# Optimization experiments

Hardware: AMD Instinct MI355X
Metric: run time of the kernel (lower is better)

The kernel has to match this reference:

```python
import jax, jax.numpy as jnp
import numpy as np

MARGIN = 0.5

def setup_inputs() -> dict:
    key = jax.random.key(0)
    k1, k2 = jax.random.split(key)
    n, d, n_classes = 8192, 512, 1024
    embedding = jax.random.normal(k1, (n, d), dtype=jnp.float32)
    label = jax.random.randint(k2, (n,), 0, n_classes, dtype=jnp.int64)
    return {"embedding": embedding, "label": label}


def reference(embedding, label):
    # sim_mat[i, j] = <e_i, e_j>
    n = embedding.shape[0]
    sim = embedding @ embedding.T  # [n, n]
    same = label[:, None] == label[None, :]  # [n, n] bool
    # per-row positive pairs: same label AND sim < 1; loss contrib (1 - sim)
    pos_mask = same & (sim < 1.0)
    # per-row negative pairs (hard mining): diff label AND sim > margin; loss contrib sim
    neg_mask = (~same) & (sim > MARGIN)
    pos_loss = jnp.sum(jnp.where(pos_mask, 1.0 - sim, 0.0))
    neg_loss = jnp.sum(jnp.where(neg_mask, sim, 0.0))
    loss = (pos_loss + neg_loss) / n
    return (loss, 0, 0)
```

## Files before the change

### kernel.cpp

```cpp
#include <hip/hip_runtime.h>
#include <hip/hip_bf16.h>


typedef int   i32x4 __attribute__((ext_vector_type(4)));
typedef float f32x4 __attribute__((ext_vector_type(4)));

#define N_EMB 8192
#define D_EMB 512
#define BM    128
#define HKB   64
#define NPH   (D_EMB / HKB)
#define TILES (N_EMB / BM)
#define NBLK  (TILES * (TILES + 1) / 2)
#define MARGIN_F 0.5f
#define QSCALE 24.0f
#define DEQ    (1.0f / (QSCALE * QSCALE))
#define HBYT  (BM * HKB)

__device__ __forceinline__ void gll16(const void* g, void* l) {
    __builtin_amdgcn_global_load_lds(
        (const __attribute__((address_space(1))) void*)g,
        (__attribute__((address_space(3))) void*)l,
        16 , 0 , 0 );
}

__global__ __launch_bounds__(256) void quant_kernel(const float* __restrict__ in,
                                                    int4* __restrict__ out, int n16) {
    int i = blockIdx.x * blockDim.x + threadIdx.x;
    if (i >= n16) return;
    const float4* p = reinterpret_cast<const float4*>(in) + i * 4;
    int4 o;
    int* po = reinterpret_cast<int*>(&o);
#pragma unroll
    for (int j = 0; j < 4; ++j) {
        float4 v = p[j];
        int b0 = (int)rintf(fminf(fmaxf(v.x * QSCALE, -127.f), 127.f));
        int b1 = (int)rintf(fminf(fmaxf(v.y * QSCALE, -127.f), 127.f));
        int b2 = (int)rintf(fminf(fmaxf(v.z * QSCALE, -127.f), 127.f));
        int b3 = (int)rintf(fminf(fmaxf(v.w * QSCALE, -127.f), 127.f));
        po[j] = (b0 & 255) | ((b1 & 255) << 8) | ((b2 & 255) << 16) | ((b3 & 255) << 24);
    }
    out[i] = o;
}

__global__ __launch_bounds__(256) void loss_kernel(const char* __restrict__ E8,
                                                   const int* __restrict__ label,
                                                   float* __restrict__ partials) {
    const int bid = blockIdx.x;
    const int t = (bid & 7) * (NBLK / 8) + (bid >> 3);

    int tr = (int)(64.5f - sqrtf(4160.25f - 2.0f * (float)t));
    while ((tr + 1) * TILES - ((tr + 1) * tr) / 2 <= t) ++tr;
    while (tr * TILES - (tr * (tr - 1)) / 2 > t) --tr;
    const int tc = tr + (t - (tr * TILES - (tr * (tr - 1)) / 2));

    __shared__ char  lds[3][2][HBYT];
    __shared__ float red[4];

    const int tid  = threadIdx.x;
    const int wid  = tid >> 6, lane = tid & 63;
    const int wrow = wid >> 1, wcol = wid & 1;
    const int fr   = lane & 15;
    const int kq   = lane >> 4;
    const int row0 = tr * BM, col0 = tc * BM;

    const int sw = (((tid & 3) ^ ((tid >> 2) & 3)) << 4);
    const int r0 = tid >> 2, r1 = 64 + (tid >> 2);
    const char* gA0 = E8 + (size_t)(row0 + r0) * D_EMB + sw;
    const char* gA1 = E8 + (size_t)(row0 + r1) * D_EMB + sw;
    const char* gB0 = E8 + (size_t)(col0 + r0) * D_EMB + sw;
    const char* gB1 = E8 + (size_t)(col0 + r1) * D_EMB + sw;
    const int d0 = tid << 4;
    const int d1 = (tid + 256) << 4;

    i32x4 acc[4][4] = {};

    const int psw = ((kq ^ (fr & 3)) << 4);

    gll16(gA0,       &lds[0][0][d0]); gll16(gA1,       &lds[0][0][d1]);
    gll16(gB0,       &lds[0][1][d0]); gll16(gB1,       &lds[0][1][d1]);
    gll16(gA0 + HKB, &lds[1][0][d0]); gll16(gA1 + HKB, &lds[1][0][d1]);
    gll16(gB0 + HKB, &lds[1][1][d0]); gll16(gB1 + HKB, &lds[1][1][d1]);
    asm volatile("s_waitcnt vmcnt(4)" ::: "memory");
    __builtin_amdgcn_s_barrier();

#pragma unroll
    for (int p = 0; p < NPH; ++p) {
        const int rg = p % 3;
        i32x4 a[4], b[4];
#pragma unroll
        for (int m = 0; m < 4; ++m)
            a[m] = *reinterpret_cast<const i32x4*>(
                &lds[rg][0][((wrow * 64 + m * 16 + fr) << 6) + psw]);
#pragma unroll
        for (int n = 0; n < 4; ++n)
            b[n] = *reinterpret_cast<const i32x4*>(
                &lds[rg][1][((wcol * 64 + n * 16 + fr) << 6) + psw]);
        if (p + 2 < NPH) {
            const int rg2 = (p + 2) % 3;
            const int ko  = (p + 2) * HKB;
            gll16(gA0 + ko, &lds[rg2][0][d0]); gll16(gA1 + ko, &lds[rg2][0][d1]);
            gll16(gB0 + ko, &lds[rg2][1][d0]); gll16(gB1 + ko, &lds[rg2][1][d1]);
        }
        if (p < NPH - 2) {
            asm volatile("s_waitcnt vmcnt(4)" ::: "memory");
        } else if (p == NPH - 2) {
            asm volatile("s_waitcnt vmcnt(0)" ::: "memory");
        }
        __builtin_amdgcn_s_barrier();
        asm volatile("s_waitcnt lgkmcnt(0)" ::: "memory");
        __builtin_amdgcn_sched_barrier(0);
        __builtin_amdgcn_s_setprio(1);
#pragma unroll
        for (int m = 0; m < 4; ++m)
#pragma unroll
            for (int n = 0; n < 4; ++n)
                acc[m][n] = __builtin_amdgcn_mfma_i32_16x16x64_i8(a[m], b[n], acc[m][n], 0, 0, 0);
        __builtin_amdgcn_s_setprio(0);
        __builtin_amdgcn_s_barrier();
    }

    float local = 0.f;
    int lj[4];
#pragma unroll
    for (int n = 0; n < 4; ++n) lj[n] = label[col0 + wcol * 64 + n * 16 + fr];
    const int rb = kq << 2;
#pragma unroll
    for (int m = 0; m < 4; ++m) {
#pragma unroll
        for (int r = 0; r < 4; ++r) {
            const int li = label[row0 + wrow * 64 + m * 16 + rb + r];
#pragma unroll
            for (int n = 0; n < 4; ++n) {
                const float s = (float)acc[m][n][r] * DEQ;
                if (li == lj[n]) {
                    if (s < 1.0f) local += 1.0f - s;
                } else if (s > MARGIN_F) {
                    local += s;
                }
            }
        }
    }
    if (tr != tc) local *= 2.0f;

#pragma unroll
    for (int off = 32; off > 0; off >>= 1) local += __shfl_xor(local, off);
    if (lane == 0) red[wid] = local;
    __syncthreads();
    if (tid == 0) partials[t] = red[0] + red[1] + red[2] + red[3];
}

__global__ __launch_bounds__(256) void reduce_kernel(const float* __restrict__ partials,
                                                     float* __restrict__ out, int nb) {
    float s = 0.f;
    for (int i = threadIdx.x; i < nb; i += 256) s += partials[i];
#pragma unroll
    for (int off = 32; off > 0; off >>= 1) s += __shfl_xor(s, off);
    __shared__ float red[4];
    if ((threadIdx.x & 63) == 0) red[threadIdx.x >> 6] = s;
    __syncthreads();
    if (threadIdx.x == 0) {
        out[0] = (red[0] + red[1] + red[2] + red[3]) * (1.0f / (float)N_EMB);
        out[1] = 0.f;
        out[2] = 0.f;
    }
}

extern "C" void kernel_launch(void* const* d_in, const int* in_sizes, int n_in,
                              void* d_out, int out_size, void* d_ws, size_t ws_size,
                              hipStream_t stream) {
    const float* emb   = (const float*)d_in[0];
    const int*   label = (const int*)d_in[1];
    float*       out   = (float*)d_out;

    char*  E8      = (char*)d_ws;
    float* partial = (float*)((char*)d_ws + (size_t)N_EMB * D_EMB);

    const int n16 = N_EMB * D_EMB / 16;
    quant_kernel<<<(n16 + 255) / 256, 256, 0, stream>>>(emb, (int4*)E8, n16);

    loss_kernel<<<NBLK, 256, 0, stream>>>(E8, label, partial);

    reduce_kernel<<<1, 256, 0, stream>>>(partial, out, NBLK);
}
```

Baseline: 46.15 us.

## Use 256x128 rectangular tiles with 512-thread blocks and per-element triangle masking

The loss kernel moves from square 128x128 upper-triangle tiles to 256-row by 128-column tiles run by 8 waves, with a new row/column tile mapping over the triangle. Each block loads a larger A panel that all 8 waves share, which cuts global and LDS load traffic per output element. Diagonal tiles are now handled by masking to gi<gj and doubling each term, instead of doubling whole off-diagonal tiles. This wastes some MFMA work on the partly covered diagonal tiles and drops the i==j terms, which only matters if a self-similarity is below 1. The larger LDS footprint may also lower occupancy.

New measurement: 47.26 us. 1.02x slower.

```diff
diff --git a/kernel.cpp b/kernel.cpp
--- a/kernel.cpp
+++ b/kernel.cpp
@@ -7,15 +7,18 @@
 
 #define N_EMB 8192
 #define D_EMB 512
-#define BM    128
+#define BMR   256
+#define BNC   128
 #define HKB   64
 #define NPH   (D_EMB / HKB)
-#define TILES (N_EMB / BM)
-#define NBLK  (TILES * (TILES + 1) / 2)
+#define RT    (N_EMB / BMR)
+#define CT    (N_EMB / BNC)
+#define NBLK  1056
 #define MARGIN_F 0.5f
 #define QSCALE 24.0f
 #define DEQ    (1.0f / (QSCALE * QSCALE))
-#define HBYT  (BM * HKB)
+#define ABYT  (BMR * HKB)
+#define BBYT  (BNC * HKB)
 
 __device__ __forceinline__ void gll16(const void* g, void* l) {
     __builtin_amdgcn_global_load_lds(
@@ -43,45 +46,46 @@
     out[i] = o;
 }
 
-__global__ __launch_bounds__(256) void loss_kernel(const char* __restrict__ E8,
+__global__ __launch_bounds__(512) void loss_kernel(const char* __restrict__ E8,
                                                    const int* __restrict__ label,
                                                    float* __restrict__ partials) {
     const int bid = blockIdx.x;
     const int t = (bid & 7) * (NBLK / 8) + (bid >> 3);
 
-    int tr = (int)(64.5f - sqrtf(4160.25f - 2.0f * (float)t));
-    while ((tr + 1) * TILES - ((tr + 1) * tr) / 2 <= t) ++tr;
-    while (tr * TILES - (tr * (tr - 1)) / 2 > t) --tr;
-    const int tc = tr + (t - (tr * TILES - (tr * (tr - 1)) / 2));
+    int R = (int)((65.0f - sqrtf(4225.0f - 4.0f * (float)t)) * 0.5f);
+    if (R < 0) R = 0; if (R > RT - 1) R = RT - 1;
+    while ((R + 1) * (65 - (R + 1)) <= t) ++R;
+    while (R * (65 - R) > t) --R;
+    const int C = 2 * R + (t - R * (65 - R));
 
-    __shared__ char  lds[3][2][HBYT];
-    __shared__ float red[4];
+    __shared__ char  lds[3][ABYT + BBYT];
+    __shared__ float red[8];
 
     const int tid  = threadIdx.x;
     const int wid  = tid >> 6, lane = tid & 63;
     const int wrow = wid >> 1, wcol = wid & 1;
     const int fr   = lane & 15;
     const int kq   = lane >> 4;
-    const int row0 = tr * BM, col0 = tc * BM;
+    const int row0 = R * BMR, col0 = C * BNC;
 
-    const int sw = (((tid & 3) ^ ((tid >> 2) & 3)) << 4);
-    const int r0 = tid >> 2, r1 = 64 + (tid >> 2);
+    const int sw  = (((tid & 3) ^ ((tid >> 2) & 3)) << 4);
+    const int r0  = tid >> 2;
     const char* gA0 = E8 + (size_t)(row0 + r0) * D_EMB + sw;
-    const char* gA1 = E8 + (size_t)(row0 + r1) * D_EMB + sw;
-    const char* gB0 = E8 + (size_t)(col0 + r0) * D_EMB + sw;
-    const char* gB1 = E8 + (size_t)(col0 + r1) * D_EMB + sw;
-    const int d0 = tid << 4;
-    const int d1 = (tid + 256) << 4;
+    const char* gA1 = E8 + (size_t)(row0 + 128 + r0) * D_EMB + sw;
+    const char* gB  = E8 + (size_t)(col0 + r0) * D_EMB + sw;
+    const int dA0 = tid << 4;
+    const int dA1 = (tid + 512) << 4;
+    const int dB  = ABYT + (tid << 4);
 
     i32x4 acc[4][4] = {};
 
     const int psw = ((kq ^ (fr & 3)) << 4);
 
-    gll16(gA0,       &lds[0][0][d0]); gll16(gA1,       &lds[0][0][d1]);
-    gll16(gB0,       &lds[0][1][d0]); gll16(gB1,       &lds[0][1][d1]);
-    gll16(gA0 + HKB, &lds[1][0][d0]); gll16(gA1 + HKB, &lds[1][0][d1]);
-    gll16(gB0 + HKB, &lds[1][1][d0]); gll16(gB1 + HKB, &lds[1][1][d1]);
-    asm volatile("s_waitcnt vmcnt(4)" ::: "memory");
+    gll16(gA0,       &lds[0][dA0]); gll16(gA1,       &lds[0][dA1]);
+    gll16(gB,        &lds[0][dB]);
+    gll16(gA0 + HKB, &lds[1][dA0]); gll16(gA1 + HKB, &lds[1][dA1]);
+    gll16(gB  + HKB, &lds[1][dB]);
+    asm volatile("s_waitcnt vmcnt(3)" ::: "memory");
     __builtin_amdgcn_s_barrier();
 
 #pragma unroll
@@ -91,19 +95,19 @@
 #pragma unroll
         for (int m = 0; m < 4; ++m)
             a[m] = *reinterpret_cast<const i32x4*>(
-                &lds[rg][0][((wrow * 64 + m * 16 + fr) << 6) + psw]);
+                &lds[rg][((wrow * 64 + m * 16 + fr) << 6) + psw]);
 #pragma unroll
         for (int n = 0; n < 4; ++n)
             b[n] = *reinterpret_cast<const i32x4*>(
-                &lds[rg][1][((wcol * 64 + n * 16 + fr) << 6) + psw]);
+                &lds[rg][ABYT + ((wcol * 64 + n * 16 + fr) << 6) + psw]);
         if (p + 2 < NPH) {
             const int rg2 = (p + 2) % 3;
             const int ko  = (p + 2) * HKB;
-            gll16(gA0 + ko, &lds[rg2][0][d0]); gll16(gA1 + ko, &lds[rg2][0][d1]);
-            gll16(gB0 + ko, &lds[rg2][1][d0]); gll16(gB1 + ko, &lds[rg2][1][d1]);
+            gll16(gA0 + ko, &lds[rg2][dA0]); gll16(gA1 + ko, &lds[rg2][dA1]);
+            gll16(gB  + ko, &lds[rg2][dB]);
         }
         if (p < NPH - 2) {
-            asm volatile("s_waitcnt vmcnt(4)" ::: "memory");
+            asm volatile("s_waitcnt vmcnt(3)" ::: "memory");
         } else if (p == NPH - 2) {
             asm volatile("s_waitcnt vmcnt(0)" ::: "memory");
         }
@@ -129,25 +133,33 @@
     for (int m = 0; m < 4; ++m) {
 #pragma unroll
         for (int r = 0; r < 4; ++r) {
-            const int li = label[row0 + wrow * 64 + m * 16 + rb + r];
+            const int gi = row0 + wrow * 64 + m * 16 + rb + r;
+            const int li = label[gi];
 #pragma unroll
             for (int n = 0; n < 4; ++n) {
+                const int gj = col0 + wcol * 64 + n * 16 + fr;
                 const float s = (float)acc[m][n][r] * DEQ;
+                float term = 0.f;
                 if (li == lj[n]) {
-                    if (s < 1.0f) local += 1.0f - s;
+                    if (s < 1.0f) term = 1.0f - s;
                 } else if (s > MARGIN_F) {
-                    local += s;
+                    term = s;
                 }
+                local += (gi < gj) ? 2.0f * term : 0.f;
             }
         }
     }
-    if (tr != tc) local *= 2.0f;
 
 #pragma unroll
     for (int off = 32; off > 0; off >>= 1) local += __shfl_xor(local, off);
     if (lane == 0) red[wid] = local;
     __syncthreads();
-    if (tid == 0) partials[t] = red[0] + red[1] + red[2] + red[3];
+    if (tid == 0) {
+        float s = 0.f;
+#pragma unroll
+        for (int i = 0; i < 8; ++i) s += red[i];
+        partials[t] = s;
+    }
 }
 
 __global__ __launch_bounds__(256) void reduce_kernel(const float* __restrict__ partials,
@@ -179,7 +191,7 @@
     const int n16 = N_EMB * D_EMB / 16;
     quant_kernel<<<(n16 + 255) / 256, 256, 0, stream>>>(emb, (int4*)E8, n16);
 
-    loss_kernel<<<NBLK, 256, 0, stream>>>(E8, label, partial);
+    loss_kernel<<<NBLK, 512, 0, stream>>>(E8, label, partial);
 
     reduce_kernel<<<1, 256, 0, stream>>>(partial, out, NBLK);
 }
```

## Deepen LDS pipeline to four stages and prefetch next fragments into registers

Applied to the files above, without the earlier changes.

The shared-memory ring grows from three to four stages, so global-to-LDS loads run three phases ahead. LDS fragment reads for the next phase are now issued before the current phase's MFMAs and held in a second register set, which overlaps LDS latency with matrix math. This also cuts one barrier per iteration. The cost is more LDS (64KB) and more VGPRs, which may reduce occupancy, and the hand-tuned vmcnt/lgkmcnt waits have to stay correct.

Result: slower. 56.49 us (+22.4%).

```diff
diff --git a/kernel.cpp b/kernel.cpp
--- a/kernel.cpp
+++ b/kernel.cpp
@@ -3,7 +3,6 @@
 
 
 typedef int   i32x4 __attribute__((ext_vector_type(4)));
-typedef float f32x4 __attribute__((ext_vector_type(4)));
 
 #define N_EMB 8192
 #define D_EMB 512
@@ -15,7 +14,7 @@
 #define MARGIN_F 0.5f
 #define QSCALE 24.0f
 #define DEQ    (1.0f / (QSCALE * QSCALE))
-#define HBYT  (BM * HKB)
+#define OBYT  8192
 
 __device__ __forceinline__ void gll16(const void* g, void* l) {
     __builtin_amdgcn_global_load_lds(
@@ -54,7 +53,7 @@
     while (tr * TILES - (tr * (tr - 1)) / 2 > t) --tr;
     const int tc = tr + (t - (tr * TILES - (tr * (tr - 1)) / 2));
 
-    __shared__ char  lds[3][2][HBYT];
+    __shared__ char  lds[4][2 * OBYT];
     __shared__ float red[4];
 
     const int tid  = threadIdx.x;
@@ -77,47 +76,71 @@
 
     const int psw = ((kq ^ (fr & 3)) << 4);
 
-    gll16(gA0,       &lds[0][0][d0]); gll16(gA1,       &lds[0][0][d1]);
-    gll16(gB0,       &lds[0][1][d0]); gll16(gB1,       &lds[0][1][d1]);
-    gll16(gA0 + HKB, &lds[1][0][d0]); gll16(gA1 + HKB, &lds[1][0][d1]);
-    gll16(gB0 + HKB, &lds[1][1][d0]); gll16(gB1 + HKB, &lds[1][1][d1]);
+#pragma unroll
+    for (int q = 0; q < 3; ++q) {
+        char* w = lds[q];
+        const int ko = q * HKB;
+        gll16(gA0 + ko, w + d0);        gll16(gA1 + ko, w + d1);
+        gll16(gB0 + ko, w + OBYT + d0); gll16(gB1 + ko, w + OBYT + d1);
+    }
+    asm volatile("s_waitcnt vmcnt(8)" ::: "memory");
+    __builtin_amdgcn_s_barrier();
+
+    i32x4 ac[4], bc[4];
+#pragma unroll
+    for (int m = 0; m < 4; ++m)
+        ac[m] = *reinterpret_cast<const i32x4*>(
+            &lds[0][((wrow * 64 + m * 16 + fr) << 6) + psw]);
+#pragma unroll
+    for (int n = 0; n < 4; ++n)
+        bc[n] = *reinterpret_cast<const i32x4*>(
+            &lds[0][OBYT + ((wcol * 64 + n * 16 + fr) << 6) + psw]);
     asm volatile("s_waitcnt vmcnt(4)" ::: "memory");
     __builtin_amdgcn_s_barrier();
 
 #pragma unroll
     for (int p = 0; p < NPH; ++p) {
-        const int rg = p % 3;
-        i32x4 a[4], b[4];
-#pragma unroll
-        for (int m = 0; m < 4; ++m)
-            a[m] = *reinterpret_cast<const i32x4*>(
-                &lds[rg][0][((wrow * 64 + m * 16 + fr) << 6) + psw]);
-#pragma unroll
-        for (int n = 0; n < 4; ++n)
-            b[n] = *reinterpret_cast<const i32x4*>(
-                &lds[rg][1][((wcol * 64 + n * 16 + fr) << 6) + psw]);
-        if (p + 2 < NPH) {
-            const int rg2 = (p + 2) % 3;
-            const int ko  = (p + 2) * HKB;
-            gll16(gA0 + ko, &lds[rg2][0][d0]); gll16(gA1 + ko, &lds[rg2][0][d1]);
-            gll16(gB0 + ko, &lds[rg2][1][d0]); gll16(gB1 + ko, &lds[rg2][1][d1]);
-        }
-        if (p < NPH - 2) {
-            asm volatile("s_waitcnt vmcnt(4)" ::: "memory");
-        } else if (p == NPH - 2) {
-            asm volatile("s_waitcnt vmcnt(0)" ::: "memory");
-        }
-        __builtin_amdgcn_s_barrier();
-        asm volatile("s_waitcnt lgkmcnt(0)" ::: "memory");
+        if (p + 3 < NPH) {
+            char* w = lds[(p + 3) & 3];
+            const int ko = (p + 3) * HKB;
+            gll16(gA0 + ko, w + d0);        gll16(gA1 + ko, w + d1);
+            gll16(gB0 + ko, w + OBYT + d0); gll16(gB1 + ko, w + OBYT + d1);
+        }
+        i32x4 an[4], bn[4];
+        if (p + 1 < NPH) {
+            const char* rdb = lds[(p + 1) & 3];
+#pragma unroll
+            for (int m = 0; m < 4; ++m)
+                an[m] = *reinterpret_cast<const i32x4*>(
+                    &rdb[((wrow * 64 + m * 16 + fr) << 6) + psw]);
+#pragma unroll
+            for (int n = 0; n < 4; ++n)
+                bn[n] = *reinterpret_cast<const i32x4*>(
+                    &rdb[OBYT + ((wcol * 64 + n * 16 + fr) << 6) + psw]);
+            asm volatile("s_waitcnt lgkmcnt(8)" ::: "memory");
+        } else {
+            asm volatile("s_waitcnt lgkmcnt(0)" ::: "memory");
+        }
         __builtin_amdgcn_sched_barrier(0);
         __builtin_amdgcn_s_setprio(1);
 #pragma unroll
         for (int m = 0; m < 4; ++m)
 #pragma unroll
             for (int n = 0; n < 4; ++n)
-                acc[m][n] = __builtin_amdgcn_mfma_i32_16x16x64_i8(a[m], b[n], acc[m][n], 0, 0, 0);
+                acc[m][n] = __builtin_amdgcn_mfma_i32_16x16x64_i8(ac[m], bc[n], acc[m][n], 0, 0, 0);
         __builtin_amdgcn_s_setprio(0);
-        __builtin_amdgcn_s_barrier();
+        if (p <= 4) {
+            asm volatile("s_waitcnt vmcnt(4)" ::: "memory");
+        } else if (p == 5) {
+            asm volatile("s_waitcnt vmcnt(0)" ::: "memory");
+        }
+        if (p < NPH - 2) __builtin_amdgcn_s_barrier();
+        if (p + 1 < NPH) {
+#pragma unroll
+            for (int m = 0; m < 4; ++m) ac[m] = an[m];
+#pragma unroll
+            for (int n = 0; n < 4; ++n) bc[n] = bn[n];
+        }
     }
 
     float local = 0.f;
```
